# Performance work log

Measured on AMD Instinct MI355X. Metric: run time of the kernel, lower is better.

The kernel has to match this reference:

```python
import jax, jax.numpy as jnp
import numpy as np

C, G = 512, 16            # channels, groups
GC = C // G               # group channels = 32
OFFSET_SCALE = 1.0
EPS = 1e-6


def setup_inputs() -> dict:
    key = jax.random.key(0)
    ks = jax.random.split(key, 4)
    N, H, W = 8, 64, 64
    return {
        "input_first": jax.random.normal(ks[0], (N, C, H, W), jnp.float32),
        "input_last": jax.random.normal(ks[1], (N, H, W, C), jnp.float32),
        "dw_w": jax.random.normal(ks[2], (C, 1, 3, 3), jnp.float32) * 0.1,  # depthwise kernel (OIHW, I=1)
        "dw_b": jnp.zeros((C,), jnp.float32),
        "ln_g": jnp.ones((C,), jnp.float32),
        "ln_b": jnp.zeros((C,), jnp.float32),
        "off_w": jax.random.normal(ks[3], (2 * G, C), jnp.float32) * 0.02,  # nonzero (module zero-inits)
        "off_b": jnp.zeros((2 * G,), jnp.float32),
    }


def _bilinear(img, px, py):
    # align_corners=False, padding_mode='zeros'.
    Hin, Win, _ = img.shape
    x0 = jnp.floor(px)
    y0 = jnp.floor(py)
    wx1 = px - x0
    wy1 = py - y0

    def tap(xi, yi, w):
        xc = jnp.clip(xi, 0, Win - 1).astype(jnp.int32)
        yc = jnp.clip(yi, 0, Hin - 1).astype(jnp.int32)
        valid = ((xi >= 0) & (xi <= Win - 1) & (yi >= 0) & (yi <= Hin - 1)).astype(img.dtype)
        return img[yc, xc] * (w * valid)[:, None]  # [L, GC]

    return (tap(x0, y0, (1 - wx1) * (1 - wy1)) + tap(x0 + 1, y0, wx1 * (1 - wy1)) +
            tap(x0, y0 + 1, (1 - wx1) * wy1) + tap(x0 + 1, y0 + 1, wx1 * wy1))


_sampler = jax.vmap(jax.vmap(_bilinear))  # over [N, G, ...]


def _forward(input_first, input_last, dw_w, dw_b, ln_g, ln_b, off_w, off_b):
    N, _, H, W = input_first.shape
    # --- dw_conv: depthwise 3x3 conv (pad 1) -> LN (channels_last) -> GELU ---
    x = jax.lax.conv_general_dilated(
        input_first, dw_w, window_strides=(1, 1), padding='SAME',
        dimension_numbers=('NCHW', 'OIHW', 'NCHW'), feature_group_count=C)
    x = x + dw_b[None, :, None, None]
    x = jnp.transpose(x, (0, 2, 3, 1))  # NHWC
    mu = x.mean(-1, keepdims=True)
    var = x.var(-1, keepdims=True)
    x1 = (x - mu) * jax.lax.rsqrt(var + EPS) * ln_g + ln_b
    x1 = jax.nn.gelu(x1, approximate=False)

    # --- offset prediction: [N,H,W, G*2], pairs are (x, y) per DCNv3 layout ---
    off = jnp.einsum('nhwc,oc->nhwo', x1, off_w) + off_b
    off = off.reshape(N, H, W, G, 2)

    # --- DCNv3 core, kernel_size=1, pad=0, stride=1, dilation=1 ---
    # ref point = pixel center; normalized loc = (i+0.5)/size + off*scale/size;
    # grid_sample pixel coord = loc*size - 0.5 = i + off*scale.
    px = jnp.arange(W, dtype=x1.dtype)[None, None, :, None] + off[..., 0] * OFFSET_SCALE  # [N,H,W,G]
    py = jnp.arange(H, dtype=x1.dtype)[None, :, None, None] + off[..., 1] * OFFSET_SCALE
    px = px.transpose(0, 3, 1, 2).reshape(N, G, H * W)
    py = py.transpose(0, 3, 1, 2).reshape(N, G, H * W)

    img = input_last.reshape(N, H, W, G, GC).transpose(0, 3, 1, 2, 4)  # [N,G,H,W,GC]
    sampled = _sampler(img, px, py)  # [N,G,HW,GC]

    mask = jnp.ones((N, G, H * W, 1), dtype=input_last.dtype)  # mask_dcn = ones
    out = (sampled * mask).reshape(N, G, H, W, GC)
    out = out.transpose(0, 2, 3, 1, 4).reshape(N, H, W, C)
    return jnp.transpose(out, (0, 3, 1, 2))  # NCHW, as in module's final permute


def reference(input_first, input_last, dw_w, dw_b, ln_g, ln_b, off_w, off_b):
    return _forward(input_first, input_last, dw_w, dw_b, ln_g, ln_b, off_w, off_b)
```

## Files before the change

kernel.cpp:

```cpp
#include <hip/hip_runtime.h>
#include <hip/hip_bf16.h>
#include <math.h>

#define NB 8
#define CC 512
#define HH 64
#define WW 64
#define GG 16
#define GCH 32
#define OO 32
#define NGHW (NB * GG * HH * WW)
#define NPX  (NB * HH * WW)
#define XROW 520


__device__ __forceinline__ float gelu_exact(float x) {
    return 0.5f * x * (1.0f + erff(x * 0.70710678118654752f));
}

__device__ __forceinline__ unsigned pack_bf2(float a, float b) {
    __hip_bfloat162 t = __float22bfloat162_rn(make_float2(a, b));
    return *(unsigned*)&t;
}

typedef __attribute__((ext_vector_type(8))) short bf16x8;
typedef __attribute__((ext_vector_type(4))) float f32x4;

__global__ __launch_bounds__(512, 4)
void fused_conv_ln_gelu_off_kernel(const float* __restrict__ in_first,
                                   const float* __restrict__ dw_w,
                                   const float* __restrict__ dw_b,
                                   const float* __restrict__ ln_g,
                                   const float* __restrict__ ln_b,
                                   const float* __restrict__ off_w,
                                   const float* __restrict__ off_b,
                                   float* __restrict__ coords)
{
    const int bid = blockIdx.x;
    const int nb  = (bid & 7) * 128 + (bid >> 3);
    const int n   = nb >> 7;
    const int h   = (nb & 127) >> 1;
    const int w0  = (nb & 1) * 32;

    const int tid  = threadIdx.x;
    const int wq   = tid & 7;
    const int cgrp = tid >> 3;
    const int wb   = wq * 4;
    const int c0   = cgrp * 8;
    const int wave = tid >> 6;
    const int lane = tid & 63;

    __shared__ short xbuf[32 * XROW];
    __shared__ float mu_s[32];
    __shared__ float rs_s[32];
    float* redS  = (float*)xbuf;
    float* redS2 = (float*)xbuf + 256;

    float xv[4][8];
    float sw[4] = {0.f, 0.f, 0.f, 0.f};
    float sq[4] = {0.f, 0.f, 0.f, 0.f};

    const float* inbase = in_first + ((size_t)n * CC + c0) * HH * WW;

    #pragma unroll
    for (int i = 0; i < 8; ++i) {
        const int c = c0 + i;
        float w9[9];
        #pragma unroll
        for (int k = 0; k < 9; ++k) w9[k] = dw_w[c * 9 + k];
        const float b = dw_b[c];
        float a0 = b, a1 = b, a2 = b, a3 = b;
        #pragma unroll
        for (int r = 0; r < 3; ++r) {
            const int y = h + r - 1;
            if (y < 0 || y >= HH) continue;
            const float* rowp0 = inbase + ((size_t)i * HH + y) * WW + w0;
            const float4 m = *(const float4*)(rowp0 + wb);
            float left  = __shfl_up(m.w, 1);
            float right = __shfl_down(m.x, 1);
            if (wq == 0) left  = (w0 > 0)       ? rowp0[-1] : 0.0f;
            if (wq == 7) right = (w0 + 32 < WW) ? rowp0[32] : 0.0f;
            const float k0 = w9[r * 3 + 0], k1 = w9[r * 3 + 1], k2 = w9[r * 3 + 2];
            a0 += k0 * left + k1 * m.x + k2 * m.y;
            a1 += k0 * m.x  + k1 * m.y + k2 * m.z;
            a2 += k0 * m.y  + k1 * m.z + k2 * m.w;
            a3 += k0 * m.z  + k1 * m.w + k2 * right;
        }
        xv[0][i] = a0; xv[1][i] = a1; xv[2][i] = a2; xv[3][i] = a3;
        sw[0] += a0; sq[0] += a0 * a0;
        sw[1] += a1; sq[1] += a1 * a1;
        sw[2] += a2; sq[2] += a2 * a2;
        sw[3] += a3; sq[3] += a3 * a3;
    }

    #pragma unroll
    for (int j = 0; j < 4; ++j) {
        sw[j] += __shfl_xor(sw[j], 8);  sq[j] += __shfl_xor(sq[j], 8);
        sw[j] += __shfl_xor(sw[j], 16); sq[j] += __shfl_xor(sq[j], 16);
        sw[j] += __shfl_xor(sw[j], 32); sq[j] += __shfl_xor(sq[j], 32);
    }
    if (lane < 8) {
        #pragma unroll
        for (int j = 0; j < 4; ++j) {
            redS [wave * 32 + wb + j] = sw[j];
            redS2[wave * 32 + wb + j] = sq[j];
        }
    }
    __syncthreads();
    if (tid < 32) {
        float s = 0.f, s2 = 0.f;
        #pragma unroll
        for (int k = 0; k < 8; ++k) {
            s  += redS [k * 32 + tid];
            s2 += redS2[k * 32 + tid];
        }
        const float mu  = s * (1.0f / 512.0f);
        const float var = s2 * (1.0f / 512.0f) - mu * mu;
        mu_s[tid] = mu;
        rs_s[tid] = rsqrtf(var + 1e-6f);
    }
    __syncthreads();

    {
        float mu_[4], rs_[4];
        #pragma unroll
        for (int j = 0; j < 4; ++j) { mu_[j] = mu_s[wb + j]; rs_[j] = rs_s[wb + j]; }
        unsigned pk[4][4];
        #pragma unroll
        for (int t = 0; t < 4; ++t) {
            const int c = c0 + 2 * t;
            const float lgA = ln_g[c],     lbA = ln_b[c];
            const float lgB = ln_g[c + 1], lbB = ln_b[c + 1];
            #pragma unroll
            for (int j = 0; j < 4; ++j) {
                const float va = (xv[j][2 * t]     - mu_[j]) * rs_[j] * lgA + lbA;
                const float vb = (xv[j][2 * t + 1] - mu_[j]) * rs_[j] * lgB + lbB;
                pk[j][t] = pack_bf2(gelu_exact(va), gelu_exact(vb));
            }
        }
        #pragma unroll
        for (int j = 0; j < 4; ++j) {
            *(uint4*)(xbuf + (size_t)(wb + j) * XROW + c0)
                = make_uint4(pk[j][0], pk[j][1], pk[j][2], pk[j][3]);
        }
    }
    __syncthreads();

    if (wave < 4) {
        const int ml   = lane & 15;
        const int quad = lane >> 4;
        const int pxT  = wave >> 1;
        const int oT   = wave & 1;

        const short* arow = xbuf + (size_t)(pxT * 16 + ml) * XROW + quad * 8;
        const float* brow = off_w + (size_t)(oT * 16 + ml) * CC + quad * 8;

        f32x4 acc = {0.f, 0.f, 0.f, 0.f};
        for (int k = 0; k < CC; k += 32) {
            const bf16x8 af = *(const bf16x8*)(arow + k);
            const float4 p = *(const float4*)(brow + k);
            const float4 q = *(const float4*)(brow + k + 4);
            union { bf16x8 v; unsigned u[4]; } bb;
            bb.u[0] = pack_bf2(p.x, p.y); bb.u[1] = pack_bf2(p.z, p.w);
            bb.u[2] = pack_bf2(q.x, q.y); bb.u[3] = pack_bf2(q.z, q.w);
            acc = __builtin_amdgcn_mfma_f32_16x16x32_bf16(af, bb.v, acc, 0, 0, 0);
        }

        const int   o   = oT * 16 + ml;
        const float ob  = off_b[o];
        const int   par = o & 1;
        const int   g   = o >> 1;
        #pragma unroll
        for (int r = 0; r < 4; ++r) {
            const int w = w0 + pxT * 16 + quad * 4 + r;
            const float base = par ? (float)h : (float)w;
            coords[(size_t)par * NGHW + (((size_t)n * GG + g) * HH + h) * WW + w]
                = base + acc[r] + ob;
        }
    }
}

__global__ __launch_bounds__(256)
void sample_kernel(const float* __restrict__ in_last,
                   const float* __restrict__ coord_ws,
                   float* __restrict__ out)
{
    const int bid = blockIdx.x;
    const int nb  = (bid & 7) * 1024 + (bid >> 3);
    const int h   = nb & 63;
    const int n   = (nb >> 6) & 7;
    const int g   = nb >> 9;
    const int tid = threadIdx.x;

    __shared__ float pxs[64];
    __shared__ float pys[64];
    __shared__ float smem[64 * 33];

    if (tid < 128) {
        const int w = tid & 63;
        const size_t cidx = (((size_t)n * GG + g) * HH + h) * WW + w;
        if (tid < 64) pxs[w] = coord_ws[cidx];
        else          pys[w] = coord_ws[cidx + NGHW];
    }
    __syncthreads();

    const int c4    = tid & 7;
    const int wslot = tid >> 3;
    const float* base = in_last + (size_t)n * HH * WW * CC + g * GCH + c4 * 4;

    int   off[8];
    float wt [8];
    #pragma unroll
    for (int p = 0; p < 2; ++p) {
        const int w = wslot + p * 32;
        const float px = pxs[w];
        const float py = pys[w];
        const float x0f = floorf(px), y0f = floorf(py);
        const float fx = px - x0f, fy = py - y0f;
        const int x0 = (int)x0f, y0 = (int)y0f;
        #pragma unroll
        for (int t = 0; t < 4; ++t) {
            const int xi = x0 + (t & 1);
            const int yi = y0 + (t >> 1);
            const int xc = min(max(xi, 0), WW - 1);
            const int yc = min(max(yi, 0), HH - 1);
            const float valid = (xi >= 0 && xi < WW && yi >= 0 && yi < HH) ? 1.0f : 0.0f;
            wt [p * 4 + t] = ((t & 1) ? fx : 1.0f - fx) * ((t >> 1) ? fy : 1.0f - fy) * valid;
            off[p * 4 + t] = (yc * WW + xc) * CC;
        }
    }
    float4 v[8];
    #pragma unroll
    for (int i = 0; i < 8; ++i) v[i] = *(const float4*)(base + off[i]);

    float4 a0 = make_float4(0.f, 0.f, 0.f, 0.f);
    float4 a1 = make_float4(0.f, 0.f, 0.f, 0.f);
    #pragma unroll
    for (int t = 0; t < 4; ++t) {
        a0.x += wt[t] * v[t].x;     a0.y += wt[t] * v[t].y;
        a0.z += wt[t] * v[t].z;     a0.w += wt[t] * v[t].w;
        a1.x += wt[4 + t] * v[4 + t].x; a1.y += wt[4 + t] * v[4 + t].y;
        a1.z += wt[4 + t] * v[4 + t].z; a1.w += wt[4 + t] * v[4 + t].w;
    }
    {
        float* sp0 = smem + wslot * 33 + c4 * 4;
        float* sp1 = smem + (wslot + 32) * 33 + c4 * 4;
        sp0[0] = a0.x; sp0[1] = a0.y; sp0[2] = a0.z; sp0[3] = a0.w;
        sp1[0] = a1.x; sp1[1] = a1.y; sp1[2] = a1.z; sp1[3] = a1.w;
    }
    __syncthreads();

    const int c  = tid >> 4;
    const int w4 = (tid & 15) * 4;
    #pragma unroll
    for (int p = 0; p < 2; ++p) {
        const int cc = c + p * 16;
        f32x4 o;
        o.x = smem[(w4 + 0) * 33 + cc];
        o.y = smem[(w4 + 1) * 33 + cc];
        o.z = smem[(w4 + 2) * 33 + cc];
        o.w = smem[(w4 + 3) * 33 + cc];
        __builtin_nontemporal_store(
            o, (f32x4*)(out + (((size_t)n * CC + g * GCH + cc) * HH + h) * WW + w4));
    }
}

extern "C" void kernel_launch(void* const* d_in, const int* in_sizes, int n_in,
                              void* d_out, int out_size, void* d_ws, size_t ws_size,
                              hipStream_t stream) {
    const float* in_first = (const float*)d_in[0];
    const float* in_last  = (const float*)d_in[1];
    const float* dw_w     = (const float*)d_in[2];
    const float* dw_b     = (const float*)d_in[3];
    const float* ln_g     = (const float*)d_in[4];
    const float* ln_b     = (const float*)d_in[5];
    const float* off_w    = (const float*)d_in[6];
    const float* off_b    = (const float*)d_in[7];
    float* out = (float*)d_out;

    float* coord_ws = (float*)d_ws;

    fused_conv_ln_gelu_off_kernel<<<HH * 2 * NB, 512, 0, stream>>>(
        in_first, dw_w, dw_b, ln_g, ln_b, off_w, off_b, coord_ws);

    sample_kernel<<<HH * NB * GG, 256, 0, stream>>>(in_last, coord_ws, out);
}
```

Before: 243.0 us.

## Fuse bilinear sampling into conv/LN/offset kernel, drop coord workspace round-trip

Merges the offset-prediction kernel and the sampling kernel into a single kernel. Each block keeps its 16 groups x 32 pixels of sampling coordinates in shared memory and then gathers from input_last, transposing through the reused xbuf before storing NCHW output. This removes the global coordinate write and read and one kernel launch. In exchange, the sampling phase now runs inside a 512-thread block with high LDS usage and extra barriers, which may lower occupancy and memory-level parallelism during the gather.

```diff
diff --git a/kernel.cpp b/kernel.cpp
--- a/kernel.cpp
+++ b/kernel.cpp
@@ -9,10 +9,7 @@
 #define GG 16
 #define GCH 32
 #define OO 32
-#define NGHW (NB * GG * HH * WW)
-#define NPX  (NB * HH * WW)
 #define XROW 520
-
 
 __device__ __forceinline__ float gelu_exact(float x) {
     return 0.5f * x * (1.0f + erff(x * 0.70710678118654752f));
@@ -27,14 +24,15 @@
 typedef __attribute__((ext_vector_type(4))) float f32x4;
 
 __global__ __launch_bounds__(512, 4)
-void fused_conv_ln_gelu_off_kernel(const float* __restrict__ in_first,
-                                   const float* __restrict__ dw_w,
-                                   const float* __restrict__ dw_b,
-                                   const float* __restrict__ ln_g,
-                                   const float* __restrict__ ln_b,
-                                   const float* __restrict__ off_w,
-                                   const float* __restrict__ off_b,
-                                   float* __restrict__ coords)
+void fused_all_kernel(const float* __restrict__ in_first,
+                      const float* __restrict__ in_last,
+                      const float* __restrict__ dw_w,
+                      const float* __restrict__ dw_b,
+                      const float* __restrict__ ln_g,
+                      const float* __restrict__ ln_b,
+                      const float* __restrict__ off_w,
+                      const float* __restrict__ off_b,
+                      float* __restrict__ out)
 {
     const int bid = blockIdx.x;
     const int nb  = (bid & 7) * 128 + (bid >> 3);
@@ -53,6 +51,8 @@
     __shared__ short xbuf[32 * XROW];
     __shared__ float mu_s[32];
     __shared__ float rs_s[32];
+    __shared__ float pxs_l[GG][32];
+    __shared__ float pys_l[GG][32];
     float* redS  = (float*)xbuf;
     float* redS2 = (float*)xbuf + 256;
 
@@ -170,54 +170,34 @@
         const float ob  = off_b[o];
         const int   par = o & 1;
         const int   g   = o >> 1;
+        float* dst = par ? &pys_l[0][0] : &pxs_l[0][0];
         #pragma unroll
         for (int r = 0; r < 4; ++r) {
-            const int w = w0 + pxT * 16 + quad * 4 + r;
-            const float base = par ? (float)h : (float)w;
-            coords[(size_t)par * NGHW + (((size_t)n * GG + g) * HH + h) * WW + w]
-                = base + acc[r] + ob;
-        }
-    }
-}
-
-__global__ __launch_bounds__(256)
-void sample_kernel(const float* __restrict__ in_last,
-                   const float* __restrict__ coord_ws,
-                   float* __restrict__ out)
-{
-    const int bid = blockIdx.x;
-    const int nb  = (bid & 7) * 1024 + (bid >> 3);
-    const int h   = nb & 63;
-    const int n   = (nb >> 6) & 7;
-    const int g   = nb >> 9;
-    const int tid = threadIdx.x;
-
-    __shared__ float pxs[64];
-    __shared__ float pys[64];
-    __shared__ float smem[64 * 33];
-
-    if (tid < 128) {
-        const int w = tid & 63;
-        const size_t cidx = (((size_t)n * GG + g) * HH + h) * WW + w;
-        if (tid < 64) pxs[w] = coord_ws[cidx];
-        else          pys[w] = coord_ws[cidx + NGHW];
-    }
-    __syncthreads();
-
-    const int c4    = tid & 7;
-    const int wslot = tid >> 3;
-    const float* base = in_last + (size_t)n * HH * WW * CC + g * GCH + c4 * 4;
-
-    int   off[8];
-    float wt [8];
-    #pragma unroll
-    for (int p = 0; p < 2; ++p) {
-        const int w = wslot + p * 32;
-        const float px = pxs[w];
-        const float py = pys[w];
-        const float x0f = floorf(px), y0f = floorf(py);
-        const float fx = px - x0f, fy = py - y0f;
+            const int wl = pxT * 16 + quad * 4 + r;
+            const float base = par ? (float)h : (float)(w0 + wl);
+            dst[g * 32 + wl] = base + acc[r] + ob;
+        }
+    }
+    __syncthreads();
+
+    float* smem = (float*)xbuf;
+    const int g4  = tid >> 7;
+    const int spx = (tid >> 2) & 31;
+    const int sc4 = tid & 3;
+    const int cl  = tid >> 2;
+    const int q   = tid & 3;
+    const float* sbase = in_last + (size_t)n * HH * WW * CC;
+
+    for (int gp = 0; gp < 4; ++gp) {
+        const int g = gp * 4 + g4;
+        const float ppx = pxs_l[g][spx];
+        const float ppy = pys_l[g][spx];
+        const float x0f = floorf(ppx), y0f = floorf(ppy);
+        const float fx = ppx - x0f, fy = ppy - y0f;
         const int x0 = (int)x0f, y0 = (int)y0f;
+
+        int   off[4];
+        float wt [4];
         #pragma unroll
         for (int t = 0; t < 4; ++t) {
             const int xi = x0 + (t & 1);
@@ -225,43 +205,44 @@
             const int xc = min(max(xi, 0), WW - 1);
             const int yc = min(max(yi, 0), HH - 1);
             const float valid = (xi >= 0 && xi < WW && yi >= 0 && yi < HH) ? 1.0f : 0.0f;
-            wt [p * 4 + t] = ((t & 1) ? fx : 1.0f - fx) * ((t >> 1) ? fy : 1.0f - fy) * valid;
-            off[p * 4 + t] = (yc * WW + xc) * CC;
-        }
-    }
-    float4 v[8];
-    #pragma unroll
-    for (int i = 0; i < 8; ++i) v[i] = *(const float4*)(base + off[i]);
-
-    float4 a0 = make_float4(0.f, 0.f, 0.f, 0.f);
-    float4 a1 = make_float4(0.f, 0.f, 0.f, 0.f);
-    #pragma unroll
-    for (int t = 0; t < 4; ++t) {
-        a0.x += wt[t] * v[t].x;     a0.y += wt[t] * v[t].y;
-        a0.z += wt[t] * v[t].z;     a0.w += wt[t] * v[t].w;
-        a1.x += wt[4 + t] * v[4 + t].x; a1.y += wt[4 + t] * v[4 + t].y;
-        a1.z += wt[4 + t] * v[4 + t].z; a1.w += wt[4 + t] * v[4 + t].w;
-    }
-    {
-        float* sp0 = smem + wslot * 33 + c4 * 4;
-        float* sp1 = smem + (wslot + 32) * 33 + c4 * 4;
-        sp0[0] = a0.x; sp0[1] = a0.y; sp0[2] = a0.z; sp0[3] = a0.w;
-        sp1[0] = a1.x; sp1[1] = a1.y; sp1[2] = a1.z; sp1[3] = a1.w;
-    }
-    __syncthreads();
-
-    const int c  = tid >> 4;
-    const int w4 = (tid & 15) * 4;
-    #pragma unroll
-    for (int p = 0; p < 2; ++p) {
-        const int cc = c + p * 16;
-        f32x4 o;
-        o.x = smem[(w4 + 0) * 33 + cc];
-        o.y = smem[(w4 + 1) * 33 + cc];
-        o.z = smem[(w4 + 2) * 33 + cc];
-        o.w = smem[(w4 + 3) * 33 + cc];
-        __builtin_nontemporal_store(
-            o, (f32x4*)(out + (((size_t)n * CC + g * GCH + cc) * HH + h) * WW + w4));
+            wt [t] = ((t & 1) ? fx : 1.0f - fx) * ((t >> 1) ? fy : 1.0f - fy) * valid;
+            off[t] = (yc * WW + xc) * CC;
+        }
+        const float* tb = sbase + g * GCH + sc4 * 8;
+        float4 v[8];
+        #pragma unroll
+        for (int t = 0; t < 4; ++t) {
+            v[2 * t]     = *(const float4*)(tb + off[t]);
+            v[2 * t + 1] = *(const float4*)(tb + off[t] + 4);
+        }
+        float a[8] = {0.f, 0.f, 0.f, 0.f, 0.f, 0.f, 0.f, 0.f};
+        #pragma unroll
+        for (int t = 0; t < 4; ++t) {
+            a[0] += wt[t] * v[2 * t].x;     a[1] += wt[t] * v[2 * t].y;
+            a[2] += wt[t] * v[2 * t].z;     a[3] += wt[t] * v[2 * t].w;
+            a[4] += wt[t] * v[2 * t + 1].x; a[5] += wt[t] * v[2 * t + 1].y;
+            a[6] += wt[t] * v[2 * t + 1].z; a[7] += wt[t] * v[2 * t + 1].w;
+        }
+        __syncthreads();
+        {
+            const int row = g4 * 32 + spx;
+            #pragma unroll
+            for (int j = 0; j < 8; ++j) smem[row * 33 + sc4 * 8 + j] = a[j];
+        }
+        __syncthreads();
+        {
+            const int g4r = cl >> 5;
+            const int cin = cl & 31;
+            const int c   = (gp * 4 + g4r) * GCH + cin;
+            float o[8];
+            #pragma unroll
+            for (int j = 0; j < 8; ++j) o[j] = smem[(g4r * 32 + q * 8 + j) * 33 + cin];
+            f32x4 o1 = {o[0], o[1], o[2], o[3]};
+            f32x4 o2 = {o[4], o[5], o[6], o[7]};
+            float* op = out + (((size_t)n * CC + c) * HH + h) * WW + w0 + q * 8;
+            __builtin_nontemporal_store(o1, (f32x4*)op);
+            __builtin_nontemporal_store(o2, (f32x4*)(op + 4));
+        }
     }
 }
 
@@ -277,11 +258,8 @@
     const float* off_w    = (const float*)d_in[6];
     const float* off_b    = (const float*)d_in[7];
     float* out = (float*)d_out;
-
-    float* coord_ws = (float*)d_ws;
-
-    fused_conv_ln_gelu_off_kernel<<<HH * 2 * NB, 512, 0, stream>>>(
-        in_first, dw_w, dw_b, ln_g, ln_b, off_w, off_b, coord_ws);
-
-    sample_kernel<<<HH * NB * GG, 256, 0, stream>>>(in_last, coord_ws, out);
-}
+    (void)d_ws; (void)ws_size;
+
+    fused_all_kernel<<<HH * 2 * NB, 512, 0, stream>>>(
+        in_first, in_last, dw_w, dw_b, ln_g, ln_b, off_w, off_b, out);
+}
```

New measurement: 248.2 us. 1.02x slower.
